# Kernel optimization log

Measured on AMD Instinct MI355X. Metric: run time of the kernel, lower is better.

The kernel has to match this reference:

```python
import jax, jax.numpy as jnp
import numpy as np

DIM = 256
HEADS = 4
HEAD_DIM = DIM // HEADS          # 64
KEY_DIM = HEAD_DIM // 2          # 32 (attn_ratio=0.5)
HIDDEN = DIM + 2 * KEY_DIM * HEADS  # 512
B, H, W = 2, 64, 64
EPS = 1e-5


def _conv2d(x, w, groups=1, pad=0):
    return jax.lax.conv_general_dilated(
        x, w, window_strides=(1, 1), padding=[(pad, pad), (pad, pad)],
        dimension_numbers=('NCHW', 'OIHW', 'NCHW'), feature_group_count=groups)


def _bn(x, g, b, m, v):
    scale = g / jnp.sqrt(v + EPS)
    return x * scale[None, :, None, None] + (b - m * scale)[None, :, None, None]


def setup_inputs() -> dict:
    key = jax.random.key(0)
    ks = jax.random.split(key, 16)
    d = {
        'x': jax.random.normal(ks[0], (B, DIM, H, W), jnp.float32),
        'qkv_w': jax.random.normal(ks[1], (HIDDEN, DIM, 1, 1), jnp.float32) * 0.05,
        'qkv_g': jax.random.uniform(ks[2], (HIDDEN,), jnp.float32, 0.5, 1.5),
        'qkv_b': jax.random.normal(ks[3], (HIDDEN,), jnp.float32) * 0.1,
        'qkv_m': jax.random.normal(ks[4], (HIDDEN,), jnp.float32) * 0.1,
        'qkv_v': jax.random.uniform(ks[5], (HIDDEN,), jnp.float32, 0.5, 1.5),
        'proj_w': jax.random.normal(ks[6], (DIM, DIM, 1, 1), jnp.float32) * 0.05,
        'proj_g': jax.random.uniform(ks[7], (DIM,), jnp.float32, 0.5, 1.5),
        'proj_b': jax.random.normal(ks[8], (DIM,), jnp.float32) * 0.1,
        'proj_m': jax.random.normal(ks[9], (DIM,), jnp.float32) * 0.1,
        'proj_v': jax.random.uniform(ks[10], (DIM,), jnp.float32, 0.5, 1.5),
        'pe_w': jax.random.normal(ks[11], (DIM, 1, 3, 3), jnp.float32) * 0.1,
        'pe_g': jax.random.uniform(ks[12], (DIM,), jnp.float32, 0.5, 1.5),
        'pe_b': jax.random.normal(ks[13], (DIM,), jnp.float32) * 0.1,
        'pe_m': jax.random.normal(ks[14], (DIM,), jnp.float32) * 0.1,
        'pe_v': jax.random.uniform(ks[15], (DIM,), jnp.float32, 0.5, 1.5),
    }
    return d


def reference(x, qkv_w, qkv_g, qkv_b, qkv_m, qkv_v,
              proj_w, proj_g, proj_b, proj_m, proj_v,
              pe_w, pe_g, pe_b, pe_m, pe_v):
    b, c, h, w = x.shape
    n = h * w
    scale = KEY_DIM ** -0.5

    qkv = _bn(_conv2d(x, qkv_w), qkv_g, qkv_b, qkv_m, qkv_v)  # [b, hidden, h, w]
    qkv = qkv.reshape(b, HEADS, 2 * KEY_DIM + HEAD_DIM, n)
    q = qkv[:, :, :KEY_DIM]                       # [b, heads, key_dim, n]
    k = qkv[:, :, KEY_DIM:2 * KEY_DIM]            # [b, heads, key_dim, n]
    v = qkv[:, :, 2 * KEY_DIM:]                   # [b, heads, head_dim, n]

    # attn[b,h,i,j] = sum_d q[b,h,d,i] * k[b,h,d,j] * scale; softmax over j
    attn = jnp.einsum('bhdi,bhdj->bhij', q, k) * scale
    attn = jax.nn.softmax(attn, axis=-1)

    # y = v @ attn^T : out[b,h,d,i] = sum_j v[b,h,d,j] * attn[b,h,i,j]
    y = jnp.einsum('bhdj,bhij->bhdi', v, attn).reshape(b, c, h, w)

    pe = _bn(_conv2d(v.reshape(b, c, h, w), pe_w, groups=c, pad=1),
             pe_g, pe_b, pe_m, pe_v)
    y = y + pe
    return _bn(_conv2d(y, proj_w), proj_g, proj_b, proj_m, proj_v)
```

## Files before the change

### kernel.cpp

```cpp
#include <hip/hip_runtime.h>
#include <hip/hip_bf16.h>

#define NSP 4096
#define BEPS 1e-5f
#define JSPLIT 4
#define JCHUNK (NSP / JSPLIT)

using short8  = __attribute__((ext_vector_type(8))) short;
using half8   = __attribute__((ext_vector_type(8))) _Float16;
using f32x4   = __attribute__((ext_vector_type(4))) float;

#define SCALE_LOG2E 0.2550348883f

__device__ __forceinline__ float b2f(unsigned short u) {
  return __uint_as_float(((unsigned)u) << 16);
}
__device__ __forceinline__ float b2f_lo(unsigned w) {
  return __uint_as_float(w << 16);
}
__device__ __forceinline__ float b2f_hi(unsigned w) {
  return __uint_as_float(w & 0xffff0000u);
}
__device__ __forceinline__ unsigned short f2b(float x) {
  unsigned u = __float_as_uint(x);
  u += 0x7fffu + ((u >> 16) & 1u);
  return (unsigned short)(u >> 16);
}
__device__ __forceinline__ unsigned pk_bf16(float a, float b) {
  return ((unsigned)f2b(b) << 16) | (unsigned)f2b(a);
}
__device__ __forceinline__ unsigned pk2u(float a, float b) {
  __hip_bfloat162 h = __float22bfloat162_rn(float2{a, b});
  unsigned r;
  __builtin_memcpy(&r, &h, sizeof(r));
  return r;
}
__device__ __forceinline__ unsigned short f2h(float x) {
  _Float16 h = (_Float16)x;
  unsigned short u;
  __builtin_memcpy(&u, &h, sizeof(u));
  return u;
}
__device__ __forceinline__ unsigned pk_h2(float a, float b) {
  return ((unsigned)f2h(b) << 16) | (unsigned)f2h(a);
}

__global__ __launch_bounds__(256) void cast_w_kernel(
    const float* __restrict__ qkv_w, const float* __restrict__ proj_w,
    unsigned short* __restrict__ wqb, unsigned short* __restrict__ wpb)
{
  const int i = blockIdx.x * 256 + threadIdx.x;
  if (i < 131072)       wqb[i] = f2h(qkv_w[i]);
  else                  wpb[i - 131072] = f2b(proj_w[i - 131072]);
}

__global__ __launch_bounds__(256) void transpose_x_kernel(
    const float* __restrict__ x, unsigned short* __restrict__ xT)
{
  const int n0 = blockIdx.x * 64, c0 = blockIdx.y * 64, b = blockIdx.z;
  __shared__ __align__(16) unsigned short tx[64][72];
  const int t = threadIdx.x;
  const int row = t >> 2;
  const int seg = t & 3;
  {
    const float* xp = x + ((size_t)(b * 256 + c0 + row)) * NSP + n0 + seg * 16;
    #pragma unroll
    for (int q4 = 0; q4 < 4; ++q4) {
      const float4 a = *reinterpret_cast<const float4*>(xp + q4 * 4);
      tx[seg * 16 + q4 * 4 + 0][row] = f2h(a.x);
      tx[seg * 16 + q4 * 4 + 1][row] = f2h(a.y);
      tx[seg * 16 + q4 * 4 + 2][row] = f2h(a.z);
      tx[seg * 16 + q4 * 4 + 3][row] = f2h(a.w);
    }
  }
  __syncthreads();
  const int nrow = t >> 2, ch = t & 3;
  unsigned short* op = xT + ((size_t)(b * NSP + n0 + nrow)) * 256 + c0 + ch * 16;
  *reinterpret_cast<float4*>(op)     = *reinterpret_cast<const float4*>(&tx[nrow][ch * 16]);
  *reinterpret_cast<float4*>(op + 8) = *reinterpret_cast<const float4*>(&tx[nrow][ch * 16 + 8]);
}

__global__ __launch_bounds__(256) void qkv_gemm_kernel(
    const unsigned short* __restrict__ xT, const unsigned short* __restrict__ wqb,
    const float* __restrict__ gg, const float* __restrict__ bb,
    const float* __restrict__ mm, const float* __restrict__ vv,
    unsigned short* __restrict__ qb, unsigned short* __restrict__ kb,
    unsigned short* __restrict__ vb)
{
  const int n0 = blockIdx.x * 128;
  const int cotile = blockIdx.y;
  const int b = blockIdx.z;
  const int co0 = cotile * 64;
  const int t = threadIdx.x;
  __shared__ __align__(16) unsigned short wt[64][136];
  __shared__ __align__(16) unsigned short xt[128][136];
  const int lane = t & 63, wave = t >> 6;
  const int m16 = lane & 15, quad = lane >> 4;

  f32x4 acc[8] = {};
  for (int kc = 0; kc < 2; ++kc) {
    if (kc) __syncthreads();
    {
      const unsigned short* wp = wqb + (size_t)(co0 + (t >> 2)) * 256 + kc * 128 + (t & 3) * 32;
      #pragma unroll
      for (int u = 0; u < 4; ++u)
        *reinterpret_cast<float4*>(&wt[t >> 2][(t & 3) * 32 + u * 8]) =
            *reinterpret_cast<const float4*>(wp + u * 8);
      const unsigned short* xp = xT + ((size_t)(b * NSP + n0 + (t >> 1))) * 256 + kc * 128 + (t & 1) * 64;
      #pragma unroll
      for (int u = 0; u < 8; ++u)
        *reinterpret_cast<float4*>(&xt[t >> 1][(t & 1) * 64 + u * 8]) =
            *reinterpret_cast<const float4*>(xp + u * 8);
    }
    __syncthreads();
    if ((cotile & 1) == 0) {
      #pragma unroll
      for (int ks = 0; ks < 4; ++ks) {
        const half8 af = *reinterpret_cast<const half8*>(&wt[wave * 16 + m16][ks * 32 + quad * 8]);
        #pragma unroll
        for (int nt = 0; nt < 8; ++nt) {
          const half8 bf = *reinterpret_cast<const half8*>(&xt[nt * 16 + m16][ks * 32 + quad * 8]);
          acc[nt] = __builtin_amdgcn_mfma_f32_16x16x32_f16(af, bf, acc[nt], 0, 0, 0);
        }
      }
    } else {
      #pragma unroll
      for (int ks = 0; ks < 4; ++ks) {
        const half8 bf = *reinterpret_cast<const half8*>(&wt[wave * 16 + m16][ks * 32 + quad * 8]);
        #pragma unroll
        for (int nt = 0; nt < 8; ++nt) {
          const half8 af = *reinterpret_cast<const half8*>(&xt[nt * 16 + m16][ks * 32 + quad * 8]);
          acc[nt] = __builtin_amdgcn_mfma_f32_16x16x32_f16(af, bf, acc[nt], 0, 0, 0);
        }
      }
    }
  }

  const int head = cotile >> 1;
  const int bh = b * 4 + head;
  if ((cotile & 1) == 0) {
    const int coh = wave * 16 + quad * 4;
    const bool isq = (coh < 32);
    const float fold = isq ? SCALE_LOG2E : 1.0f;
    float sc[4], bi[4];
    #pragma unroll
    for (int r = 0; r < 4; ++r) {
      const int c = co0 + coh + r;
      const float s0 = gg[c] * rsqrtf(vv[c] + BEPS);
      sc[r] = s0 * fold;
      bi[r] = (bb[c] - mm[c] * s0) * fold;
    }
    unsigned short* dst = isq ? qb : kb;
    const int d0 = coh & 31;
    #pragma unroll
    for (int nt = 0; nt < 8; ++nt) {
      const int i = n0 + nt * 16 + m16;
      uint2 pk2;
      pk2.x = pk_h2(acc[nt][0] * sc[0] + bi[0], acc[nt][1] * sc[1] + bi[1]);
      pk2.y = pk_h2(acc[nt][2] * sc[2] + bi[2], acc[nt][3] * sc[3] + bi[3]);
      *reinterpret_cast<uint2*>(dst + ((size_t)bh * NSP + i) * 32 + d0) = pk2;
    }
  } else {
    const int c = co0 + wave * 16 + m16;
    const float sc = gg[c] * rsqrtf(vv[c] + BEPS);
    const float bi = bb[c] - mm[c] * sc;
    const int d = wave * 16 + m16;
    #pragma unroll
    for (int nt = 0; nt < 8; ++nt) {
      const int j = n0 + nt * 16 + quad * 4;
      uint2 pk2;
      pk2.x = pk_bf16(acc[nt][0] * sc + bi, acc[nt][1] * sc + bi);
      pk2.y = pk_bf16(acc[nt][2] * sc + bi, acc[nt][3] * sc + bi);
      *reinterpret_cast<uint2*>(vb + ((size_t)(bh * 64 + d)) * NSP + j) = pk2;
    }
  }
}

__global__ __launch_bounds__(256, 4) void attn_kernel(
    const unsigned short* __restrict__ qb, const unsigned short* __restrict__ kb,
    const unsigned short* __restrict__ vb,
    unsigned short* __restrict__ Opart, float* __restrict__ lpart)
{
  const int i0    = blockIdx.x * 128;
  const int bh    = blockIdx.y;
  const int split = blockIdx.z;
  const int jbase = split * JCHUNK;
  const int t  = threadIdx.x;
  const int lane = t & 63, wave = t >> 6;
  const int m16 = lane & 15, quad = lane >> 4;
  __shared__ __align__(16) short smem[16384];
  short (*qs)[40] = (short(*)[40])smem;
  short (*ps)[72] = (short(*)[72])smem;
  short (*ks)[40] = (short(*)[40])(smem + 9216);
  short (*vs)[72] = (short(*)[72])(smem + 9216 + 2560);

  {
    const unsigned short* qp = qb + ((size_t)bh * NSP + i0) * 32;
    const int r = t >> 1, h = t & 1;
    *reinterpret_cast<float4*>(&qs[r][h * 16]) =
        *reinterpret_cast<const float4*>(qp + r * 32 + h * 16);
    *reinterpret_cast<float4*>(&qs[r][h * 16 + 8]) =
        *reinterpret_cast<const float4*>(qp + r * 32 + h * 16 + 8);
  }
  __syncthreads();
  half8 qfrag[2];
  qfrag[0] = *reinterpret_cast<const half8*>(&qs[wave * 32 + m16][quad * 8]);
  qfrag[1] = *reinterpret_cast<const half8*>(&qs[wave * 32 + 16 + m16][quad * 8]);

  float rsum[2] = {0.f, 0.f};
  f32x4 oacc[2][4] = {};

  const int srow = t >> 2, schunk = t & 3;
  const unsigned short* kbase = kb + (size_t)bh * NSP * 32;
  const unsigned short* vbase = vb + (size_t)bh * 64 * NSP;

  float4 kreg, vreg0, vreg1;
  kreg  = *reinterpret_cast<const float4*>(kbase + (size_t)(jbase + srow) * 32 + schunk * 8);
  vreg0 = *reinterpret_cast<const float4*>(vbase + (size_t)srow * NSP + jbase + schunk * 16);
  vreg1 = *reinterpret_cast<const float4*>(vbase + (size_t)srow * NSP + jbase + schunk * 16 + 8);
  *reinterpret_cast<float4*>(&ks[srow][schunk * 8]) = kreg;
  *reinterpret_cast<float4*>(&vs[srow][schunk * 16]) = vreg0;
  *reinterpret_cast<float4*>(&vs[srow][schunk * 16 + 8]) = vreg1;
  __syncthreads();

  for (int jt0 = 0; jt0 < JCHUNK; jt0 += 64) {
    const bool more = (jt0 + 64) < JCHUNK;
    if (more) {
      const int jn = jbase + jt0 + 64;
      kreg  = *reinterpret_cast<const float4*>(kbase + (size_t)(jn + srow) * 32 + schunk * 8);
      vreg0 = *reinterpret_cast<const float4*>(vbase + (size_t)srow * NSP + jn + schunk * 16);
      vreg1 = *reinterpret_cast<const float4*>(vbase + (size_t)srow * NSP + jn + schunk * 16 + 8);
    }

    half8 kf[4];
    #pragma unroll
    for (int jt = 0; jt < 4; ++jt)
      kf[jt] = *reinterpret_cast<const half8*>(&ks[jt * 16 + m16][quad * 8]);

    #pragma unroll
    for (int it = 0; it < 2; ++it) {
      f32x4 sacc[4];
      #pragma unroll
      for (int jt = 0; jt < 4; ++jt)
        sacc[jt] = __builtin_amdgcn_mfma_f32_16x16x32_f16(kf[jt], qfrag[it],
                                                          (f32x4){0.f,0.f,0.f,0.f}, 0, 0, 0);
      const int irow = wave * 32 + it * 16 + m16;
      #pragma unroll
      for (int jt = 0; jt < 4; ++jt) {
        float p0 = __builtin_amdgcn_exp2f(sacc[jt][0]);
        float p1 = __builtin_amdgcn_exp2f(sacc[jt][1]);
        float p2 = __builtin_amdgcn_exp2f(sacc[jt][2]);
        float p3 = __builtin_amdgcn_exp2f(sacc[jt][3]);
        rsum[it] += (p0 + p1) + (p2 + p3);
        uint2 pk2;
        pk2.x = pk2u(p0, p1);
        pk2.y = pk2u(p2, p3);
        *reinterpret_cast<uint2*>(&ps[irow][jt * 16 + quad * 4]) = pk2;
      }
    }

    short8 pa[2][2];
    #pragma unroll
    for (int it = 0; it < 2; ++it) {
      pa[it][0] = *reinterpret_cast<const short8*>(&ps[wave * 32 + it * 16 + m16][quad * 8]);
      pa[it][1] = *reinterpret_cast<const short8*>(&ps[wave * 32 + it * 16 + m16][32 + quad * 8]);
    }
    #pragma unroll
    for (int dt = 0; dt < 4; ++dt) {
      const short8 v0 = *reinterpret_cast<const short8*>(&vs[dt * 16 + m16][quad * 8]);
      const short8 v1 = *reinterpret_cast<const short8*>(&vs[dt * 16 + m16][32 + quad * 8]);
      #pragma unroll
      for (int it = 0; it < 2; ++it) {
        oacc[it][dt] = __builtin_amdgcn_mfma_f32_16x16x32_bf16(pa[it][0], v0, oacc[it][dt], 0, 0, 0);
        oacc[it][dt] = __builtin_amdgcn_mfma_f32_16x16x32_bf16(pa[it][1], v1, oacc[it][dt], 0, 0, 0);
      }
    }

    if (more) {
      __syncthreads();
      *reinterpret_cast<float4*>(&ks[srow][schunk * 8]) = kreg;
      *reinterpret_cast<float4*>(&vs[srow][schunk * 16]) = vreg0;
      *reinterpret_cast<float4*>(&vs[srow][schunk * 16 + 8]) = vreg1;
      __syncthreads();
    }
  }

  #pragma unroll
  for (int it = 0; it < 2; ++it) {
    float rs = rsum[it];
    rs += __shfl_xor(rs, 16);
    rs += __shfl_xor(rs, 32);
    if (quad == 0)
      lpart[((size_t)split * 8 + bh) * NSP + i0 + wave * 32 + it * 16 + m16] = rs;
  }

  #pragma unroll
  for (int it = 0; it < 2; ++it)
    #pragma unroll
    for (int dt = 0; dt < 4; ++dt) {
      const int d = dt * 16 + m16;
      uint2 pk2;
      pk2.x = pk2u(oacc[it][dt][0], oacc[it][dt][1]);
      pk2.y = pk2u(oacc[it][dt][2], oacc[it][dt][3]);
      *reinterpret_cast<uint2*>(Opart +
          (((size_t)split * 8 + bh) * 64 + d) * NSP + i0 + wave * 32 + it * 16 + quad * 4) = pk2;
    }
}

__global__ __launch_bounds__(256) void fuse_kernel(
    const unsigned short* __restrict__ Opart, const float* __restrict__ lpart,
    const unsigned short* __restrict__ vb,
    const float* __restrict__ pw, const float* __restrict__ pg,
    const float* __restrict__ pb, const float* __restrict__ pm,
    const float* __restrict__ pv,
    unsigned short* __restrict__ yT)
{
  const int py = blockIdx.x;
  const int bh = blockIdx.y;
  const int b = bh >> 2, h = bh & 3;
  const int t = threadIdx.x;
  const int d = t >> 2, seg = t & 3;
  __shared__ float lsum[64];
  __shared__ __align__(16) unsigned short yt[64][72];

  if (t < 64) {
    float ls = 0.f;
    #pragma unroll
    for (int s = 0; s < JSPLIT; ++s)
      ls += lpart[((size_t)s * 8 + bh) * NSP + py * 64 + t];
    lsum[t] = ls;
  }
  __syncthreads();

  const int c = h * 64 + d;
  const int i0 = py * 64 + seg * 16;
  float os[16] = {};
  #pragma unroll
  for (int s = 0; s < JSPLIT; ++s) {
    const uint4* op = reinterpret_cast<const uint4*>(
        Opart + (((size_t)s * 8 + bh) * 64 + d) * NSP + i0);
    const uint4 a = op[0], e = op[1];
    os[0]  += b2f_lo(a.x); os[1]  += b2f_hi(a.x);
    os[2]  += b2f_lo(a.y); os[3]  += b2f_hi(a.y);
    os[4]  += b2f_lo(a.z); os[5]  += b2f_hi(a.z);
    os[6]  += b2f_lo(a.w); os[7]  += b2f_hi(a.w);
    os[8]  += b2f_lo(e.x); os[9]  += b2f_hi(e.x);
    os[10] += b2f_lo(e.y); os[11] += b2f_hi(e.y);
    os[12] += b2f_lo(e.z); os[13] += b2f_hi(e.z);
    os[14] += b2f_lo(e.w); os[15] += b2f_hi(e.w);
  }

  float w9[9];
  #pragma unroll
  for (int i = 0; i < 9; ++i) w9[i] = pw[c * 9 + i];
  const float sc = pg[c] * rsqrtf(pv[c] + BEPS);
  const float bi = pb[c] - pm[c] * sc;
  const unsigned short* vrow = vb + ((size_t)(bh * 64 + d)) * NSP;

  float conv[16] = {};
  #pragma unroll
  for (int dy = -1; dy <= 1; ++dy) {
    const int yy = py + dy;
    if (yy < 0 || yy > 63) continue;
    const unsigned short* vr = vrow + yy * 64 + seg * 16;
    float vals[18];
    const uint4 m0 = *reinterpret_cast<const uint4*>(vr);
    const uint4 m1 = *reinterpret_cast<const uint4*>(vr + 8);
    vals[1]  = b2f_lo(m0.x); vals[2]  = b2f_hi(m0.x);
    vals[3]  = b2f_lo(m0.y); vals[4]  = b2f_hi(m0.y);
    vals[5]  = b2f_lo(m0.z); vals[6]  = b2f_hi(m0.z);
    vals[7]  = b2f_lo(m0.w); vals[8]  = b2f_hi(m0.w);
    vals[9]  = b2f_lo(m1.x); vals[10] = b2f_hi(m1.x);
    vals[11] = b2f_lo(m1.y); vals[12] = b2f_hi(m1.y);
    vals[13] = b2f_lo(m1.z); vals[14] = b2f_hi(m1.z);
    vals[15] = b2f_lo(m1.w); vals[16] = b2f_hi(m1.w);
    vals[0]  = (seg > 0) ? b2f_hi(*reinterpret_cast<const unsigned*>(vr - 2)) : 0.f;
    vals[17] = (seg < 3) ? b2f_lo(*reinterpret_cast<const unsigned*>(vr + 16)) : 0.f;
    const float wr0 = w9[(dy + 1) * 3 + 0], wr1 = w9[(dy + 1) * 3 + 1], wr2 = w9[(dy + 1) * 3 + 2];
    #pragma unroll
    for (int u = 0; u < 16; ++u)
      conv[u] += vals[u] * wr0 + vals[u + 1] * wr1 + vals[u + 2] * wr2;
  }

  #pragma unroll
  for (int u = 0; u < 16; ++u) {
    const float yv = os[u] / lsum[seg * 16 + u] + conv[u] * sc + bi;
    yt[seg * 16 + u][d] = f2b(yv);
  }
  __syncthreads();

  const int prow = t >> 2, ch = t & 3;
  unsigned short* op = yT + ((size_t)(b * NSP + py * 64 + prow)) * 256 + h * 64 + ch * 16;
  *reinterpret_cast<float4*>(op)     = *reinterpret_cast<const float4*>(&yt[prow][ch * 16]);
  *reinterpret_cast<float4*>(op + 8) = *reinterpret_cast<const float4*>(&yt[prow][ch * 16 + 8]);
}

__global__ __launch_bounds__(256) void proj_gemm_kernel(
    const unsigned short* __restrict__ yT, const unsigned short* __restrict__ wpb,
    const float* __restrict__ gg, const float* __restrict__ bb,
    const float* __restrict__ mm, const float* __restrict__ vv,
    float* __restrict__ out)
{
  const int n0 = blockIdx.x * 128;
  const int co0 = blockIdx.y * 64;
  const int b = blockIdx.z;
  const int t = threadIdx.x;
  __shared__ __align__(16) unsigned short wt[64][136];
  __shared__ __align__(16) unsigned short yt[128][136];
  const int lane = t & 63, wave = t >> 6;
  const int m16 = lane & 15, quad = lane >> 4;

  f32x4 acc[8] = {};
  for (int kc = 0; kc < 2; ++kc) {
    if (kc) __syncthreads();
    {
      const unsigned short* wp = wpb + (size_t)(co0 + (t >> 2)) * 256 + kc * 128 + (t & 3) * 32;
      #pragma unroll
      for (int u = 0; u < 4; ++u)
        *reinterpret_cast<float4*>(&wt[t >> 2][(t & 3) * 32 + u * 8]) =
            *reinterpret_cast<const float4*>(wp + u * 8);
      const unsigned short* yp = yT + ((size_t)(b * NSP + n0 + (t >> 1))) * 256 + kc * 128 + (t & 1) * 64;
      #pragma unroll
      for (int u = 0; u < 8; ++u)
        *reinterpret_cast<float4*>(&yt[t >> 1][(t & 1) * 64 + u * 8]) =
            *reinterpret_cast<const float4*>(yp + u * 8);
    }
    __syncthreads();
    #pragma unroll
    for (int ks = 0; ks < 4; ++ks) {
      const short8 bf = *reinterpret_cast<const short8*>(&wt[wave * 16 + m16][ks * 32 + quad * 8]);
      #pragma unroll
      for (int nt = 0; nt < 8; ++nt) {
        const short8 af = *reinterpret_cast<const short8*>(&yt[nt * 16 + m16][ks * 32 + quad * 8]);
        acc[nt] = __builtin_amdgcn_mfma_f32_16x16x32_bf16(af, bf, acc[nt], 0, 0, 0);
      }
    }
  }

  const int c = co0 + wave * 16 + m16;
  const float sc = gg[c] * rsqrtf(vv[c] + BEPS);
  const float bi = bb[c] - mm[c] * sc;
  #pragma unroll
  for (int nt = 0; nt < 8; ++nt) {
    const int n = n0 + nt * 16 + quad * 4;
    float4 ov;
    ov.x = acc[nt][0] * sc + bi; ov.y = acc[nt][1] * sc + bi;
    ov.z = acc[nt][2] * sc + bi; ov.w = acc[nt][3] * sc + bi;
    *reinterpret_cast<float4*>(out + ((size_t)(b * 256 + c)) * NSP + n) = ov;
  }
}

extern "C" void kernel_launch(void* const* d_in, const int* in_sizes, int n_in,
                              void* d_out, int out_size, void* d_ws, size_t ws_size,
                              hipStream_t stream)
{
  const float* x      = (const float*)d_in[0];
  const float* qkv_w  = (const float*)d_in[1];
  const float* qkv_g  = (const float*)d_in[2];
  const float* qkv_b  = (const float*)d_in[3];
  const float* qkv_m  = (const float*)d_in[4];
  const float* qkv_v  = (const float*)d_in[5];
  const float* proj_w = (const float*)d_in[6];
  const float* proj_g = (const float*)d_in[7];
  const float* proj_b = (const float*)d_in[8];
  const float* proj_m = (const float*)d_in[9];
  const float* proj_v = (const float*)d_in[10];
  const float* pe_w   = (const float*)d_in[11];
  const float* pe_g   = (const float*)d_in[12];
  const float* pe_b   = (const float*)d_in[13];
  const float* pe_m   = (const float*)d_in[14];
  const float* pe_v   = (const float*)d_in[15];
  float* out = (float*)d_out;

  unsigned short* qb = (unsigned short*)d_ws;
  unsigned short* kb = qb + (size_t)8 * NSP * 32;
  unsigned short* vb = kb + (size_t)8 * NSP * 32;
  unsigned short* Opart = vb + (size_t)8 * 64 * NSP;
  float* lpart = (float*)(Opart + (size_t)JSPLIT * 8 * 64 * NSP);
  unsigned short* xT = (unsigned short*)(lpart + (size_t)JSPLIT * 8 * NSP);
  unsigned short* yT = xT + (size_t)2 * NSP * 256;
  unsigned short* wqb = yT + (size_t)2 * NSP * 256;
  unsigned short* wpb = wqb + (size_t)512 * 256;

  cast_w_kernel<<<dim3(768), 256, 0, stream>>>(qkv_w, proj_w, wqb, wpb);
  transpose_x_kernel<<<dim3(64, 4, 2), 256, 0, stream>>>(x, xT);
  qkv_gemm_kernel<<<dim3(32, 8, 2), 256, 0, stream>>>(xT, wqb, qkv_g, qkv_b, qkv_m, qkv_v,
                                                      qb, kb, vb);
  attn_kernel<<<dim3(32, 8, JSPLIT), 256, 0, stream>>>(qb, kb, vb, Opart, lpart);
  fuse_kernel<<<dim3(64, 8), 256, 0, stream>>>(Opart, lpart, vb,
                                               pe_w, pe_g, pe_b, pe_m, pe_v, yT);
  proj_gemm_kernel<<<dim3(32, 4, 2), 256, 0, stream>>>(yT, wpb, proj_g, proj_b, proj_m, proj_v,
                                                       out);
}
```

Before: 158.8 us.

## Switch attention MFMAs to 32x32 tiles and keep P in registers

Rewrites the attention inner loop to use 32x32x16 MFMA instructions for both QK^T and PV instead of 16x16x32. The exponentiated probabilities are repacked into the A-operand layout with cross-half-wave shuffles rather than being written to and read back from shared memory. This removes the P staging buffer and its LDS traffic and cuts the instruction count, at the cost of extra shuffle/select work and larger accumulator register pressure.

```diff
diff --git a/kernel.cpp b/kernel.cpp
--- a/kernel.cpp
+++ b/kernel.cpp
@@ -9,6 +9,7 @@
 using short8  = __attribute__((ext_vector_type(8))) short;
 using half8   = __attribute__((ext_vector_type(8))) _Float16;
 using f32x4   = __attribute__((ext_vector_type(4))) float;
+using f32x16  = __attribute__((ext_vector_type(16))) float;
 
 #define SCALE_LOG2E 0.2550348883f
 
@@ -187,12 +188,11 @@
   const int jbase = split * JCHUNK;
   const int t  = threadIdx.x;
   const int lane = t & 63, wave = t >> 6;
-  const int m16 = lane & 15, quad = lane >> 4;
-  __shared__ __align__(16) short smem[16384];
-  short (*qs)[40] = (short(*)[40])smem;
-  short (*ps)[72] = (short(*)[72])smem;
-  short (*ks)[40] = (short(*)[40])(smem + 9216);
-  short (*vs)[72] = (short(*)[72])(smem + 9216 + 2560);
+  const int l31 = lane & 31, hi = lane >> 5;
+
+  __shared__ __align__(16) unsigned short qs[128][40];
+  __shared__ __align__(16) unsigned short ks[64][40];
+  __shared__ __align__(16) unsigned short vs[64][72];
 
   {
     const unsigned short* qp = qb + ((size_t)bh * NSP + i0) * 32;
@@ -202,13 +202,6 @@
     *reinterpret_cast<float4*>(&qs[r][h * 16 + 8]) =
         *reinterpret_cast<const float4*>(qp + r * 32 + h * 16 + 8);
   }
-  __syncthreads();
-  half8 qfrag[2];
-  qfrag[0] = *reinterpret_cast<const half8*>(&qs[wave * 32 + m16][quad * 8]);
-  qfrag[1] = *reinterpret_cast<const half8*>(&qs[wave * 32 + 16 + m16][quad * 8]);
-
-  float rsum[2] = {0.f, 0.f};
-  f32x4 oacc[2][4] = {};
 
   const int srow = t >> 2, schunk = t & 3;
   const unsigned short* kbase = kb + (size_t)bh * NSP * 32;
@@ -218,10 +211,19 @@
   kreg  = *reinterpret_cast<const float4*>(kbase + (size_t)(jbase + srow) * 32 + schunk * 8);
   vreg0 = *reinterpret_cast<const float4*>(vbase + (size_t)srow * NSP + jbase + schunk * 16);
   vreg1 = *reinterpret_cast<const float4*>(vbase + (size_t)srow * NSP + jbase + schunk * 16 + 8);
+
+  __syncthreads();
+  half8 qfrag[2];
+  qfrag[0] = *reinterpret_cast<const half8*>(&qs[wave * 32 + l31][hi * 8]);
+  qfrag[1] = *reinterpret_cast<const half8*>(&qs[wave * 32 + l31][16 + hi * 8]);
+
   *reinterpret_cast<float4*>(&ks[srow][schunk * 8]) = kreg;
   *reinterpret_cast<float4*>(&vs[srow][schunk * 16]) = vreg0;
   *reinterpret_cast<float4*>(&vs[srow][schunk * 16 + 8]) = vreg1;
   __syncthreads();
+
+  float rsum = 0.f;
+  f32x16 oacc[2] = {};
 
   for (int jt0 = 0; jt0 < JCHUNK; jt0 += 64) {
     const bool more = (jt0 + 64) < JCHUNK;
@@ -232,47 +234,47 @@
       vreg1 = *reinterpret_cast<const float4*>(vbase + (size_t)srow * NSP + jn + schunk * 16 + 8);
     }
 
-    half8 kf[4];
-    #pragma unroll
-    for (int jt = 0; jt < 4; ++jt)
-      kf[jt] = *reinterpret_cast<const half8*>(&ks[jt * 16 + m16][quad * 8]);
-
-    #pragma unroll
-    for (int it = 0; it < 2; ++it) {
-      f32x4 sacc[4];
-      #pragma unroll
-      for (int jt = 0; jt < 4; ++jt)
-        sacc[jt] = __builtin_amdgcn_mfma_f32_16x16x32_f16(kf[jt], qfrag[it],
-                                                          (f32x4){0.f,0.f,0.f,0.f}, 0, 0, 0);
-      const int irow = wave * 32 + it * 16 + m16;
-      #pragma unroll
-      for (int jt = 0; jt < 4; ++jt) {
-        float p0 = __builtin_amdgcn_exp2f(sacc[jt][0]);
-        float p1 = __builtin_amdgcn_exp2f(sacc[jt][1]);
-        float p2 = __builtin_amdgcn_exp2f(sacc[jt][2]);
-        float p3 = __builtin_amdgcn_exp2f(sacc[jt][3]);
-        rsum[it] += (p0 + p1) + (p2 + p3);
-        uint2 pk2;
-        pk2.x = pk2u(p0, p1);
-        pk2.y = pk2u(p2, p3);
-        *reinterpret_cast<uint2*>(&ps[irow][jt * 16 + quad * 4]) = pk2;
+    half8 kf[2][2];
+    #pragma unroll
+    for (int jt32 = 0; jt32 < 2; ++jt32) {
+      kf[jt32][0] = *reinterpret_cast<const half8*>(&ks[jt32 * 32 + l31][hi * 8]);
+      kf[jt32][1] = *reinterpret_cast<const half8*>(&ks[jt32 * 32 + l31][16 + hi * 8]);
+    }
+
+    #pragma unroll
+    for (int jt32 = 0; jt32 < 2; ++jt32) {
+      f32x16 sacc = {};
+      sacc = __builtin_amdgcn_mfma_f32_32x32x16_f16(kf[jt32][0], qfrag[0], sacc, 0, 0, 0);
+      sacc = __builtin_amdgcn_mfma_f32_32x32x16_f16(kf[jt32][1], qfrag[1], sacc, 0, 0, 0);
+
+      unsigned pk[8];
+      #pragma unroll
+      for (int c = 0; c < 8; ++c) {
+        const float p0 = __builtin_amdgcn_exp2f(sacc[2 * c]);
+        const float p1 = __builtin_amdgcn_exp2f(sacc[2 * c + 1]);
+        rsum += p0 + p1;
+        pk[c] = pk2u(p0, p1);
       }
-    }
-
-    short8 pa[2][2];
-    #pragma unroll
-    for (int it = 0; it < 2; ++it) {
-      pa[it][0] = *reinterpret_cast<const short8*>(&ps[wave * 32 + it * 16 + m16][quad * 8]);
-      pa[it][1] = *reinterpret_cast<const short8*>(&ps[wave * 32 + it * 16 + m16][32 + quad * 8]);
-    }
-    #pragma unroll
-    for (int dt = 0; dt < 4; ++dt) {
-      const short8 v0 = *reinterpret_cast<const short8*>(&vs[dt * 16 + m16][quad * 8]);
-      const short8 v1 = *reinterpret_cast<const short8*>(&vs[dt * 16 + m16][32 + quad * 8]);
-      #pragma unroll
-      for (int it = 0; it < 2; ++it) {
-        oacc[it][dt] = __builtin_amdgcn_mfma_f32_16x16x32_bf16(pa[it][0], v0, oacc[it][dt], 0, 0, 0);
-        oacc[it][dt] = __builtin_amdgcn_mfma_f32_16x16x32_bf16(pa[it][1], v1, oacc[it][dt], 0, 0, 0);
+
+      #pragma unroll
+      for (int kt = 0; kt < 2; ++kt) {
+        const unsigned s_a0 = (unsigned)__shfl_xor((int)pk[4 * kt + 0], 32);
+        const unsigned s_a1 = (unsigned)__shfl_xor((int)pk[4 * kt + 1], 32);
+        const unsigned s_b0 = (unsigned)__shfl_xor((int)pk[4 * kt + 2], 32);
+        const unsigned s_b1 = (unsigned)__shfl_xor((int)pk[4 * kt + 3], 32);
+        uint4 aw;
+        aw.x = hi ? s_b0 : pk[4 * kt + 0];
+        aw.y = hi ? s_b1 : pk[4 * kt + 1];
+        aw.z = hi ? pk[4 * kt + 2] : s_a0;
+        aw.w = hi ? pk[4 * kt + 3] : s_a1;
+        short8 af;
+        __builtin_memcpy(&af, &aw, 16);
+        #pragma unroll
+        for (int dt = 0; dt < 2; ++dt) {
+          const short8 vf = *reinterpret_cast<const short8*>(
+              &vs[dt * 32 + l31][jt32 * 32 + kt * 16 + hi * 8]);
+          oacc[dt] = __builtin_amdgcn_mfma_f32_32x32x16_bf16(af, vf, oacc[dt], 0, 0, 0);
+        }
       }
     }
 
@@ -285,26 +287,25 @@
     }
   }
 
-  #pragma unroll
-  for (int it = 0; it < 2; ++it) {
-    float rs = rsum[it];
-    rs += __shfl_xor(rs, 16);
+  {
+    float rs = rsum;
     rs += __shfl_xor(rs, 32);
-    if (quad == 0)
-      lpart[((size_t)split * 8 + bh) * NSP + i0 + wave * 32 + it * 16 + m16] = rs;
-  }
-
-  #pragma unroll
-  for (int it = 0; it < 2; ++it)
-    #pragma unroll
-    for (int dt = 0; dt < 4; ++dt) {
-      const int d = dt * 16 + m16;
+    if (hi == 0)
+      lpart[((size_t)split * 8 + bh) * NSP + i0 + wave * 32 + l31] = rs;
+  }
+
+  #pragma unroll
+  for (int dt = 0; dt < 2; ++dt) {
+    const int d = dt * 32 + l31;
+    #pragma unroll
+    for (int R = 0; R < 4; ++R) {
       uint2 pk2;
-      pk2.x = pk2u(oacc[it][dt][0], oacc[it][dt][1]);
-      pk2.y = pk2u(oacc[it][dt][2], oacc[it][dt][3]);
+      pk2.x = pk2u(oacc[dt][4 * R + 0], oacc[dt][4 * R + 1]);
+      pk2.y = pk2u(oacc[dt][4 * R + 2], oacc[dt][4 * R + 3]);
       *reinterpret_cast<uint2*>(Opart +
-          (((size_t)split * 8 + bh) * 64 + d) * NSP + i0 + wave * 32 + it * 16 + quad * 4) = pk2;
-    }
+          (((size_t)split * 8 + bh) * 64 + d) * NSP + i0 + wave * 32 + 8 * R + 4 * hi) = pk2;
+    }
+  }
 }
 
 __global__ __launch_bounds__(256) void fuse_kernel(
```

Result: no change. 158.6 us (-0.2%).
